# Kernel tuning notes

Hardware: AMD Instinct MI355X
Metric: run time of the kernel (lower is better)

## Reference

```python
import jax, jax.numpy as jnp
import numpy as np

N_NODES = 100000
N_EDGES = 1600000
IN_DIM = 128
EMB_DIM = 128
NUM_EDGE_EMB = 4
LN_EPS = 1e-5


def setup_inputs() -> dict:
    key = jax.random.key(0)
    ks = jax.random.split(key, 8)
    x = jax.random.normal(ks[0], (N_NODES, IN_DIM), dtype=jnp.float32)
    edge_index = jax.random.randint(ks[1], (2, N_EDGES), 0, N_NODES, dtype=jnp.int64)
    edge_attr = jax.random.randint(ks[2], (N_EDGES,), 0, NUM_EDGE_EMB, dtype=jnp.int64)
    # learned params
    edge_emb = jax.random.normal(ks[3], (NUM_EDGE_EMB, IN_DIM), dtype=jnp.float32)
    eps = jnp.zeros((), dtype=jnp.float32)  # GINEConv train_eps init 0
    s1 = 1.0 / np.sqrt(IN_DIM)
    W1 = jax.random.uniform(ks[4], (IN_DIM, EMB_DIM), jnp.float32, -s1, s1)
    b1 = jnp.zeros((EMB_DIM,), jnp.float32)
    ln_g = jnp.ones((EMB_DIM,), jnp.float32)
    ln_b = jnp.zeros((EMB_DIM,), jnp.float32)
    s2 = 1.0 / np.sqrt(EMB_DIM)
    W2 = jax.random.uniform(ks[5], (EMB_DIM, EMB_DIM), jnp.float32, -s2, s2)
    b2 = jnp.zeros((EMB_DIM,), jnp.float32)
    return {"x": x, "edge_index": edge_index, "edge_attr": edge_attr,
            "edge_emb": edge_emb, "eps": eps, "W1": W1, "b1": b1,
            "ln_g": ln_g, "ln_b": ln_b, "W2": W2, "b2": b2}


def reference(x, edge_index, edge_attr, edge_emb, eps, W1, b1, ln_g, ln_b, W2, b2):
    src, dst = edge_index[0], edge_index[1]
    # message: relu(x_j + e_ji), gathered per edge [E, D]
    msg = jax.nn.relu(x[src] + edge_emb[edge_attr])
    # scatter-add into destination nodes [N, D]
    agg = jax.ops.segment_sum(msg, dst, num_segments=x.shape[0])
    h = (1.0 + eps) * x + agg
    # MLP: Linear -> LayerNorm -> ReLU -> Linear
    h1 = h @ W1 + b1
    mu = jnp.mean(h1, axis=-1, keepdims=True)
    var = jnp.var(h1, axis=-1, keepdims=True)
    h1 = (h1 - mu) * jax.lax.rsqrt(var + LN_EPS) * ln_g + ln_b
    h1 = jax.nn.relu(h1)
    return h1 @ W2 + b2
```

## Files before the change

kernel.cpp:

```cpp
#include <hip/hip_runtime.h>
#include <hip/hip_fp16.h>

#define N_NODES 100000
#define N_EDGES 1600000
#define DIM 128
#define NBUK 782
#define EPB 4096
#define NBLK 391
#define NCNT (NBUK * NBLK)
#define NSC 299
#define CAPB 2720

typedef __attribute__((ext_vector_type(8))) short short8v;
typedef __attribute__((ext_vector_type(4))) float f32x4;
typedef _Float16 h2 __attribute__((ext_vector_type(2)));

__device__ __forceinline__ unsigned short f2bf(float f) {
    unsigned u = __float_as_uint(f);
    unsigned r = u + 0x7FFFu + ((u >> 16) & 1u);
    return (unsigned short)(r >> 16);
}
__device__ __forceinline__ float bf2f(unsigned short b) {
    return __uint_as_float(((unsigned)b) << 16);
}

__global__ __launch_bounds__(256) void hist2_conv(
    const int* __restrict__ ei, int* __restrict__ cnts,
    const float* __restrict__ x, ushort* __restrict__ xh, int do_conv)
{
    __shared__ int cnt[NBUK];
    for (int i = threadIdx.x; i < NBUK; i += 256) cnt[i] = 0;

    if (do_conv) {
        for (int i = blockIdx.x * 256 + threadIdx.x; i < N_NODES * DIM / 4;
             i += NBLK * 256) {
            float4 v = ((const float4*)x)[i];
            ushort4 o;
            o.x = __half_as_ushort(__float2half(v.x));
            o.y = __half_as_ushort(__float2half(v.y));
            o.z = __half_as_ushort(__float2half(v.z));
            o.w = __half_as_ushort(__float2half(v.w));
            ((ushort4*)xh)[i] = o;
        }
    }
    __syncthreads();

    int e0 = blockIdx.x * EPB;
    int e1 = min(e0 + EPB, N_EDGES);
    for (int e = e0 + threadIdx.x; e < e1; e += 256)
        atomicAdd(&cnt[ei[N_EDGES + e] >> 7], 1);
    __syncthreads();
    for (int b = threadIdx.x; b < NBUK; b += 256)
        cnts[b * NBLK + blockIdx.x] = cnt[b];
}

__global__ __launch_bounds__(256) void scanA(
    int* __restrict__ cnts, int* __restrict__ bsums)
{
    __shared__ int s[256];
    int t = threadIdx.x;
    int base = blockIdx.x * 1024 + t * 4;
    int v0 = (base + 0 < NCNT) ? cnts[base + 0] : 0;
    int v1 = (base + 1 < NCNT) ? cnts[base + 1] : 0;
    int v2 = (base + 2 < NCNT) ? cnts[base + 2] : 0;
    int v3 = (base + 3 < NCNT) ? cnts[base + 3] : 0;
    int sum = v0 + v1 + v2 + v3;
    s[t] = sum;
    __syncthreads();
    for (int off = 1; off < 256; off <<= 1) {
        int x = (t >= off) ? s[t - off] : 0;
        __syncthreads();
        s[t] += x;
        __syncthreads();
    }
    int excl = s[t] - sum;
    if (base + 0 < NCNT) cnts[base + 0] = excl;  excl += v0;
    if (base + 1 < NCNT) cnts[base + 1] = excl;  excl += v1;
    if (base + 2 < NCNT) cnts[base + 2] = excl;  excl += v2;
    if (base + 3 < NCNT) cnts[base + 3] = excl;
    if (t == 255) bsums[blockIdx.x] = s[255];
}

__global__ __launch_bounds__(512) void scanB(int* __restrict__ bsums)
{
    __shared__ int s[512];
    int t = threadIdx.x;
    int v = (t < NSC) ? bsums[t] : 0;
    s[t] = v;
    __syncthreads();
    for (int off = 1; off < 512; off <<= 1) {
        int x = (t >= off) ? s[t - off] : 0;
        __syncthreads();
        s[t] += x;
        __syncthreads();
    }
    if (t < NSC) bsums[t] = s[t] - v;
}

__global__ __launch_bounds__(256) void scanC_prepw(
    int* __restrict__ ebase, const int* __restrict__ bsums, int* __restrict__ bk,
    const float* __restrict__ W1, const float* __restrict__ W2,
    ushort* __restrict__ wf1, ushort* __restrict__ wf2)
{
    int i = blockIdx.x * 256 + threadIdx.x;
    if (i < NCNT) {
        int v = ebase[i] + bsums[i >> 10];
        ebase[i] = v;
        if (i % NBLK == 0) bk[i / NBLK] = v;
    }
    if (i == 0) bk[NBUK] = N_EDGES;

    if (i < DIM * DIM) {
        int lane = (i >> 3) & 63;
        int j = i & 7;
        int frag = i >> 9;
        int kt = frag >> 3, nt = frag & 7;
        int k = kt * 32 + (lane >> 4) * 8 + j;
        int n = nt * 16 + (lane & 15);
        wf1[i] = f2bf(W1[k * DIM + n]);
        wf2[i] = f2bf(W2[k * DIM + n]);
    }
}

__global__ __launch_bounds__(256) void pass2_scatter(
    const int* __restrict__ ei, const int* __restrict__ ea,
    const int* __restrict__ ebase, int* __restrict__ ebuf)
{
    __shared__ int cnt[NBUK];
    __shared__ int mybase[NBUK];
    for (int i = threadIdx.x; i < NBUK; i += 256) {
        cnt[i] = 0;
        mybase[i] = ebase[i * NBLK + blockIdx.x];
    }
    __syncthreads();
    int e0 = blockIdx.x * EPB;
    int e1 = min(e0 + EPB, N_EDGES);
    for (int e = e0 + threadIdx.x; e < e1; e += 256) {
        int src = ei[e];
        int dst = ei[N_EDGES + e];
        int at  = ea[e];
        int pay = src | (at << 17) | ((dst & 127) << 19);
        int b   = dst >> 7;
        int r   = atomicAdd(&cnt[b], 1);
        ebuf[mybase[b] + r] = pay;
    }
}

template<int HI>
__device__ __forceinline__ float h2acc(h2 m2, float acc) {
#if __has_builtin(__builtin_amdgcn_fdot2)
    h2 b;
    b[0] = (_Float16)(HI ? 0.f : 1.f);
    b[1] = (_Float16)(HI ? 1.f : 0.f);
    return __builtin_amdgcn_fdot2(m2, b, acc, false);
#else
    return acc + (float)m2[HI];
#endif
}

__device__ __forceinline__ void edge_acc(
    int pkv, int c, const unsigned* embh, float* acc, uint4 xv)
{
    const uint4 ev = *(const uint4*)&embh[((((unsigned)pkv >> 17) & 3) << 6) | (c << 2)];
    unsigned xs[4] = {xv.x, xv.y, xv.z, xv.w};
    unsigned es[4] = {ev.x, ev.y, ev.z, ev.w};
    const h2 z2 = (h2)(_Float16)0;
    #pragma unroll
    for (int j = 0; j < 4; ++j) {
        h2 a = __builtin_bit_cast(h2, xs[j]);
        h2 b = __builtin_bit_cast(h2, es[j]);
        h2 m2 = __builtin_elementwise_max(a + b, z2);
        acc[2 * j]     = h2acc<0>(m2, acc[2 * j]);
        acc[2 * j + 1] = h2acc<1>(m2, acc[2 * j + 1]);
    }
}

template<int USE16>
__global__ __launch_bounds__(512) void sort_gather(
    const int* __restrict__ bk, const int* __restrict__ ebuf,
    const float* __restrict__ x, const ushort* __restrict__ xh,
    const float* __restrict__ emb, const float* __restrict__ eps_p,
    ushort* __restrict__ hhi, ushort* __restrict__ hlo)
{
    __shared__ int col_l[CAPB];
    __shared__ int deg[128], sc[128], cur[128];
    __shared__ unsigned embh[256];
    __shared__ float femb[512];

    const int b = blockIdx.x;
    const int t = threadIdx.x;
    const int lo = bk[b];
    const int n_e = min(bk[b + 1] - lo, CAPB);

    if (t < 256) {
        float2 f = ((const float2*)emb)[t];
        if (USE16) {
            __half2 h = __floats2half2_rn(f.x, f.y);
            embh[t] = __builtin_bit_cast(unsigned, h);
        } else {
            femb[2 * t] = f.x;
            femb[2 * t + 1] = f.y;
        }
    }
    if (t < 128) deg[t] = 0;
    __syncthreads();

    for (int i = t; i < n_e; i += 512)
        atomicAdd(&deg[((unsigned)ebuf[lo + i] >> 19) & 127], 1);
    __syncthreads();

    if (t < 128) sc[t] = deg[t];
    __syncthreads();
    for (int off = 1; off < 128; off <<= 1) {
        int v = 0;
        if (t < 128 && t >= off) v = sc[t - off];
        __syncthreads();
        if (t < 128) sc[t] += v;
        __syncthreads();
    }
    if (t < 128) cur[t] = sc[t] - deg[t];
    __syncthreads();

    for (int i = t; i < n_e; i += 512) {
        int pk = ebuf[lo + i];
        int p = atomicAdd(&cur[((unsigned)pk >> 19) & 127], 1);
        col_l[p] = pk;
    }
    __syncthreads();

    const int g = t >> 4, c = t & 15;
    const float epsv = 1.0f + eps_p[0];

    for (int ln = g; ln < 128; ln += 32) {
        int n = b * 128 + ln;
        if (n >= N_NODES) break;
        int start = sc[ln] - deg[ln], end = sc[ln];
        float acc[8] = {0.f, 0.f, 0.f, 0.f, 0.f, 0.f, 0.f, 0.f};

        if (USE16) {
            int p = start;
            for (; p + 4 <= end; p += 4) {
                int pk[4];
                uint4 xv[4];
                #pragma unroll
                for (int u = 0; u < 4; ++u) pk[u] = col_l[p + u];
                #pragma unroll
                for (int u = 0; u < 4; ++u)
                    xv[u] = ((const uint4*)xh)[((pk[u] & 0x1FFFF) << 4) | c];
                #pragma unroll
                for (int u = 0; u < 4; ++u)
                    edge_acc(pk[u], c, embh, acc, xv[u]);
            }
            for (; p < end; ++p) {
                int pkv = col_l[p];
                uint4 xv = ((const uint4*)xh)[((pkv & 0x1FFFF) << 4) | c];
                edge_acc(pkv, c, embh, acc, xv);
            }
        } else {
            for (int p = start; p < end; ++p) {
                int pk = col_l[p];
                const float* xr = x + (size_t)(pk & 0x1FFFF) * DIM;
                float4 xa = ((const float4*)xr)[c * 2];
                float4 xb = ((const float4*)xr)[c * 2 + 1];
                const float* er = &femb[(((unsigned)pk >> 17) & 3) * DIM + c * 8];
                acc[0] += fmaxf(xa.x + er[0], 0.f);
                acc[1] += fmaxf(xa.y + er[1], 0.f);
                acc[2] += fmaxf(xa.z + er[2], 0.f);
                acc[3] += fmaxf(xa.w + er[3], 0.f);
                acc[4] += fmaxf(xb.x + er[4], 0.f);
                acc[5] += fmaxf(xb.y + er[5], 0.f);
                acc[6] += fmaxf(xb.z + er[6], 0.f);
                acc[7] += fmaxf(xb.w + er[7], 0.f);
            }
        }

        float4 xa = ((const float4*)(x + (size_t)n * DIM))[c * 2];
        float4 xb = ((const float4*)(x + (size_t)n * DIM))[c * 2 + 1];
        float o[8];
        o[0] = epsv * xa.x + acc[0];
        o[1] = epsv * xa.y + acc[1];
        o[2] = epsv * xa.z + acc[2];
        o[3] = epsv * xa.w + acc[3];
        o[4] = epsv * xb.x + acc[4];
        o[5] = epsv * xb.y + acc[5];
        o[6] = epsv * xb.z + acc[6];
        o[7] = epsv * xb.w + acc[7];

        unsigned hiw[4], low[4];
        #pragma unroll
        for (int j = 0; j < 4; ++j) {
            unsigned short h0 = f2bf(o[2 * j]);
            unsigned short h1 = f2bf(o[2 * j + 1]);
            unsigned short l0 = f2bf(o[2 * j] - bf2f(h0));
            unsigned short l1 = f2bf(o[2 * j + 1] - bf2f(h1));
            hiw[j] = (unsigned)h0 | ((unsigned)h1 << 16);
            low[j] = (unsigned)l0 | ((unsigned)l1 << 16);
        }
        ((uint4*)(hhi + (size_t)n * DIM))[c] = make_uint4(hiw[0], hiw[1], hiw[2], hiw[3]);
        ((uint4*)(hlo + (size_t)n * DIM))[c] = make_uint4(low[0], low[1], low[2], low[3]);
    }
}

__global__ __launch_bounds__(256) void fused_mlp(
    const ushort* __restrict__ hhi, const ushort* __restrict__ hlo,
    const ushort* __restrict__ wf1, const ushort* __restrict__ wf2,
    const float* __restrict__ b1,
    const float* __restrict__ lng, const float* __restrict__ lnb,
    const float* __restrict__ b2,
    float* __restrict__ out)
{
    __shared__ short w1s[DIM * DIM];
    __shared__ short w2s[DIM * DIM];
    __shared__ short scr[4 * 16 * DIM];

    #pragma unroll
    for (int i = 0; i < 8; ++i) {
        int idx = i * 256 + threadIdx.x;
        ((uint4*)w1s)[idx] = ((const uint4*)wf1)[idx];
        ((uint4*)w2s)[idx] = ((const uint4*)wf2)[idx];
    }
    __syncthreads();

    const int w  = threadIdx.x >> 6;
    const int l  = threadIdx.x & 63;
    const int lc = l & 15;
    const int lr = l >> 4;

    const int rbase = blockIdx.x * 64 + w * 16;
    const int arow = min(rbase + lc, N_NODES - 1);
    const ushort* hph = hhi + (size_t)arow * DIM;
    const ushort* hpl = hlo + (size_t)arow * DIM;

    float g[8], bb[8], bi1[8], bi2[8];
    #pragma unroll
    for (int nt = 0; nt < 8; ++nt) {
        g[nt]  = lng[nt * 16 + lc];
        bb[nt] = lnb[nt * 16 + lc];
        bi1[nt] = b1[nt * 16 + lc];
        bi2[nt] = b2[nt * 16 + lc];
    }

    f32x4 acc[8];
    #pragma unroll
    for (int nt = 0; nt < 8; ++nt)
        acc[nt] = (f32x4){bi1[nt], bi1[nt], bi1[nt], bi1[nt]};

    #pragma unroll
    for (int kt = 0; kt < 4; ++kt) {
        short8v ahi = *(const short8v*)(hph + kt * 32 + lr * 8);
        short8v alo = *(const short8v*)(hpl + kt * 32 + lr * 8);
        #pragma unroll
        for (int nt = 0; nt < 8; ++nt) {
            short8v bf = *(const short8v*)&w1s[((kt * 8 + nt) * 64 + l) * 8];
            acc[nt] = __builtin_amdgcn_mfma_f32_16x16x32_bf16(ahi, bf, acc[nt], 0, 0, 0);
            acc[nt] = __builtin_amdgcn_mfma_f32_16x16x32_bf16(alo, bf, acc[nt], 0, 0, 0);
        }
    }

    #pragma unroll
    for (int r = 0; r < 4; ++r) {
        float s1 = 0.f, s2 = 0.f;
        #pragma unroll
        for (int nt = 0; nt < 8; ++nt) { float v = acc[nt][r]; s1 += v; s2 += v * v; }
        s1 += __shfl_xor(s1, 1);  s2 += __shfl_xor(s2, 1);
        s1 += __shfl_xor(s1, 2);  s2 += __shfl_xor(s2, 2);
        s1 += __shfl_xor(s1, 4);  s2 += __shfl_xor(s2, 4);
        s1 += __shfl_xor(s1, 8);  s2 += __shfl_xor(s2, 8);
        float mu  = s1 * (1.0f / DIM);
        float var = s2 * (1.0f / DIM) - mu * mu;
        float rsd = rsqrtf(var + 1e-5f);
        int row = lr * 4 + r;
        #pragma unroll
        for (int nt = 0; nt < 8; ++nt) {
            float v = (acc[nt][r] - mu) * rsd * g[nt] + bb[nt];
            v = fmaxf(v, 0.f);
            int cidx = nt * 16 + lc;
            scr[w * 2048 + row * 128 + (((cidx >> 3) ^ row) << 3) + (cidx & 7)]
                = (short)f2bf(v);
        }
    }

    f32x4 acc2[8];
    #pragma unroll
    for (int nt = 0; nt < 8; ++nt)
        acc2[nt] = (f32x4){bi2[nt], bi2[nt], bi2[nt], bi2[nt]};

    #pragma unroll
    for (int kt = 0; kt < 4; ++kt) {
        short8v a2 = *(const short8v*)&scr[w * 2048 + lc * 128 + (((kt * 4 + lr) ^ lc) << 3)];
        #pragma unroll
        for (int nt = 0; nt < 8; ++nt) {
            short8v bf = *(const short8v*)&w2s[((kt * 8 + nt) * 64 + l) * 8];
            acc2[nt] = __builtin_amdgcn_mfma_f32_16x16x32_bf16(a2, bf, acc2[nt], 0, 0, 0);
        }
    }

    #pragma unroll
    for (int r = 0; r < 4; ++r) {
        int orow = rbase + lr * 4 + r;
        if (orow < N_NODES) {
            #pragma unroll
            for (int nt = 0; nt < 8; ++nt)
                out[(size_t)orow * DIM + nt * 16 + lc] = acc2[nt][r];
        }
    }
}

extern "C" void kernel_launch(void* const* d_in, const int* in_sizes, int n_in,
                              void* d_out, int out_size, void* d_ws, size_t ws_size,
                              hipStream_t stream) {
    const float* x    = (const float*)d_in[0];
    const int*   ei   = (const int*)d_in[1];
    const int*   ea   = (const int*)d_in[2];
    const float* emb  = (const float*)d_in[3];
    const float* epsp = (const float*)d_in[4];
    const float* W1   = (const float*)d_in[5];
    const float* b1   = (const float*)d_in[6];
    const float* lng  = (const float*)d_in[7];
    const float* lnb  = (const float*)d_in[8];
    const float* W2   = (const float*)d_in[9];
    const float* b2   = (const float*)d_in[10];
    float* out = (float*)d_out;

    char* ws = (char*)d_ws;
    int* bk     = (int*)(ws);
    int* bsums  = (int*)(ws + 4096);
    ushort* wf1 = (ushort*)(ws + 8192);
    ushort* wf2 = (ushort*)(ws + 40960);
    int* cnts   = (int*)(ws + 81920);
    int* ebuf   = (int*)(ws + 1310720);
    ushort* hhi = (ushort*)(ws + 8025984);
    ushort* hlo = (ushort*)(ws + 33625984);
    ushort* xh  = (ushort*)(ws + 59225984);
    const size_t NEED = 59225984 + (size_t)N_NODES * DIM * 2;

    const int use_f16 = (ws_size >= NEED) ? 1 : 0;

    hist2_conv<<<NBLK, 256, 0, stream>>>(ei, cnts, x, xh, use_f16);
    scanA<<<NSC, 256, 0, stream>>>(cnts, bsums);
    scanB<<<1, 512, 0, stream>>>(bsums);
    scanC_prepw<<<(NCNT + 255) / 256, 256, 0, stream>>>(
        cnts, bsums, bk, W1, W2, wf1, wf2);
    pass2_scatter<<<NBLK, 256, 0, stream>>>(ei, ea, cnts, ebuf);

    if (use_f16) {
        sort_gather<1><<<NBUK, 512, 0, stream>>>(
            bk, ebuf, x, xh, emb, epsp, hhi, hlo);
    } else {
        sort_gather<0><<<NBUK, 512, 0, stream>>>(
            bk, ebuf, x, xh, emb, epsp, hhi, hlo);
    }

    fused_mlp<<<(N_NODES + 63) / 64, 256, 0, stream>>>(
        hhi, hlo, wf1, wf2, b1, lng, lnb, b2, out);
}
```

Baseline: 158.6 us.

## Band-sort edges by source range so node groups gather with locality

The per-block counting sort now bins edges by destination node and by a 3-bit source-range band, giving 1024 bins. Each 16-thread group keeps four node accumulators in registers and walks all eight bands in order, so groups across the block read source rows from similar address ranges at the same time. The intent is better L2 locality for the random row gathers. In exchange it uses more registers (32 accumulators per thread), a longer 1024-entry scan with more barriers, and more shared memory, which may lower occupancy.

Result: slower. 178.0 us (+12.3%).

```diff
diff --git a/kernel.cpp b/kernel.cpp
--- a/kernel.cpp
+++ b/kernel.cpp
@@ -183,7 +183,9 @@
     ushort* __restrict__ hhi, ushort* __restrict__ hlo)
 {
     __shared__ int col_l[CAPB];
-    __shared__ int deg[128], sc[128], cur[128];
+    __shared__ int deg[1024];
+    __shared__ int sc[1024];
+    __shared__ int cur[1024];
     __shared__ unsigned embh[256];
     __shared__ float femb[512];
 
@@ -202,28 +204,33 @@
             femb[2 * t + 1] = f.y;
         }
     }
-    if (t < 128) deg[t] = 0;
-    __syncthreads();
-
-    for (int i = t; i < n_e; i += 512)
-        atomicAdd(&deg[((unsigned)ebuf[lo + i] >> 19) & 127], 1);
-    __syncthreads();
-
-    if (t < 128) sc[t] = deg[t];
-    __syncthreads();
-    for (int off = 1; off < 128; off <<= 1) {
-        int v = 0;
-        if (t < 128 && t >= off) v = sc[t - off];
-        __syncthreads();
-        if (t < 128) sc[t] += v;
-        __syncthreads();
-    }
-    if (t < 128) cur[t] = sc[t] - deg[t];
+    deg[t] = 0; deg[t + 512] = 0;
+    __syncthreads();
+
+    for (int i = t; i < n_e; i += 512) {
+        unsigned pk = (unsigned)ebuf[lo + i];
+        int bin = (((pk >> 19) & 127) << 3) | ((pk >> 14) & 7);
+        atomicAdd(&deg[bin], 1);
+    }
+    __syncthreads();
+
+    sc[t] = deg[t]; sc[t + 512] = deg[t + 512];
+    __syncthreads();
+    for (int off = 1; off < 1024; off <<= 1) {
+        int v0 = (t >= off) ? sc[t - off] : 0;
+        int v1 = (t + 512 >= off) ? sc[t + 512 - off] : 0;
+        __syncthreads();
+        sc[t] += v0; sc[t + 512] += v1;
+        __syncthreads();
+    }
+    cur[t] = sc[t] - deg[t];
+    cur[t + 512] = sc[t + 512] - deg[t + 512];
     __syncthreads();
 
     for (int i = t; i < n_e; i += 512) {
         int pk = ebuf[lo + i];
-        int p = atomicAdd(&cur[((unsigned)pk >> 19) & 127], 1);
+        int bin = ((((unsigned)pk >> 19) & 127) << 3) | (((unsigned)pk >> 14) & 7);
+        int p = atomicAdd(&cur[bin], 1);
         col_l[p] = pk;
     }
     __syncthreads();
@@ -231,60 +238,72 @@
     const int g = t >> 4, c = t & 15;
     const float epsv = 1.0f + eps_p[0];
 
-    for (int ln = g; ln < 128; ln += 32) {
-        int n = b * 128 + ln;
-        if (n >= N_NODES) break;
-        int start = sc[ln] - deg[ln], end = sc[ln];
-        float acc[8] = {0.f, 0.f, 0.f, 0.f, 0.f, 0.f, 0.f, 0.f};
-
-        if (USE16) {
-            int p = start;
-            for (; p + 4 <= end; p += 4) {
-                int pk[4];
-                uint4 xv[4];
-                #pragma unroll
-                for (int u = 0; u < 4; ++u) pk[u] = col_l[p + u];
-                #pragma unroll
-                for (int u = 0; u < 4; ++u)
-                    xv[u] = ((const uint4*)xh)[((pk[u] & 0x1FFFF) << 4) | c];
-                #pragma unroll
-                for (int u = 0; u < 4; ++u)
-                    edge_acc(pk[u], c, embh, acc, xv[u]);
+    float acc[4][8];
+    #pragma unroll
+    for (int q = 0; q < 4; ++q)
+        #pragma unroll
+        for (int j = 0; j < 8; ++j) acc[q][j] = 0.f;
+
+    for (int band = 0; band < 8; ++band) {
+        #pragma unroll
+        for (int q = 0; q < 4; ++q) {
+            int ln = g + q * 32;
+            int bin = ln * 8 + band;
+            int bs = sc[bin] - deg[bin], be = sc[bin];
+            if (USE16) {
+                int p = bs;
+                for (; p + 4 <= be; p += 4) {
+                    int pk[4];
+                    uint4 xv[4];
+                    #pragma unroll
+                    for (int u = 0; u < 4; ++u) pk[u] = col_l[p + u];
+                    #pragma unroll
+                    for (int u = 0; u < 4; ++u)
+                        xv[u] = ((const uint4*)xh)[((pk[u] & 0x1FFFF) << 4) | c];
+                    #pragma unroll
+                    for (int u = 0; u < 4; ++u)
+                        edge_acc(pk[u], c, embh, acc[q], xv[u]);
+                }
+                for (; p < be; ++p) {
+                    int pkv = col_l[p];
+                    uint4 xv = ((const uint4*)xh)[((pkv & 0x1FFFF) << 4) | c];
+                    edge_acc(pkv, c, embh, acc[q], xv);
+                }
+            } else {
+                for (int p = bs; p < be; ++p) {
+                    int pk = col_l[p];
+                    const float* xr = x + (size_t)(pk & 0x1FFFF) * DIM;
+                    float4 xa = ((const float4*)xr)[c * 2];
+                    float4 xb = ((const float4*)xr)[c * 2 + 1];
+                    const float* er = &femb[(((unsigned)pk >> 17) & 3) * DIM + c * 8];
+                    acc[q][0] += fmaxf(xa.x + er[0], 0.f);
+                    acc[q][1] += fmaxf(xa.y + er[1], 0.f);
+                    acc[q][2] += fmaxf(xa.z + er[2], 0.f);
+                    acc[q][3] += fmaxf(xa.w + er[3], 0.f);
+                    acc[q][4] += fmaxf(xb.x + er[4], 0.f);
+                    acc[q][5] += fmaxf(xb.y + er[5], 0.f);
+                    acc[q][6] += fmaxf(xb.z + er[6], 0.f);
+                    acc[q][7] += fmaxf(xb.w + er[7], 0.f);
+                }
             }
-            for (; p < end; ++p) {
-                int pkv = col_l[p];
-                uint4 xv = ((const uint4*)xh)[((pkv & 0x1FFFF) << 4) | c];
-                edge_acc(pkv, c, embh, acc, xv);
-            }
-        } else {
-            for (int p = start; p < end; ++p) {
-                int pk = col_l[p];
-                const float* xr = x + (size_t)(pk & 0x1FFFF) * DIM;
-                float4 xa = ((const float4*)xr)[c * 2];
-                float4 xb = ((const float4*)xr)[c * 2 + 1];
-                const float* er = &femb[(((unsigned)pk >> 17) & 3) * DIM + c * 8];
-                acc[0] += fmaxf(xa.x + er[0], 0.f);
-                acc[1] += fmaxf(xa.y + er[1], 0.f);
-                acc[2] += fmaxf(xa.z + er[2], 0.f);
-                acc[3] += fmaxf(xa.w + er[3], 0.f);
-                acc[4] += fmaxf(xb.x + er[4], 0.f);
-                acc[5] += fmaxf(xb.y + er[5], 0.f);
-                acc[6] += fmaxf(xb.z + er[6], 0.f);
-                acc[7] += fmaxf(xb.w + er[7], 0.f);
-            }
-        }
-
+        }
+    }
+
+    #pragma unroll
+    for (int q = 0; q < 4; ++q) {
+        int n = b * 128 + g + q * 32;
+        if (n >= N_NODES) continue;
         float4 xa = ((const float4*)(x + (size_t)n * DIM))[c * 2];
         float4 xb = ((const float4*)(x + (size_t)n * DIM))[c * 2 + 1];
         float o[8];
-        o[0] = epsv * xa.x + acc[0];
-        o[1] = epsv * xa.y + acc[1];
-        o[2] = epsv * xa.z + acc[2];
-        o[3] = epsv * xa.w + acc[3];
-        o[4] = epsv * xb.x + acc[4];
-        o[5] = epsv * xb.y + acc[5];
-        o[6] = epsv * xb.z + acc[6];
-        o[7] = epsv * xb.w + acc[7];
+        o[0] = epsv * xa.x + acc[q][0];
+        o[1] = epsv * xa.y + acc[q][1];
+        o[2] = epsv * xa.z + acc[q][2];
+        o[3] = epsv * xa.w + acc[q][3];
+        o[4] = epsv * xb.x + acc[q][4];
+        o[5] = epsv * xb.y + acc[q][5];
+        o[6] = epsv * xb.z + acc[q][6];
+        o[7] = epsv * xb.w + acc[q][7];
 
         unsigned hiw[4], low[4];
         #pragma unroll
```

## Enlarge histogram blocks and sub-sort bucket edges by source sub-range

Applied to the files above, without the earlier changes.

Raises edges per histogram/scatter block fourfold, which cuts the count table, the number of scan blocks and the scanB size. Inside each destination bucket, edges are now counting-sorted by destination and then by three bits of the source index (1024 bins instead of 128). Within a node's edge list, sources end up grouped by sub-range, which is meant to improve locality of the x gathers. Fewer, larger histogram blocks reduce parallelism in hist/scatter, and the sub-sort adds a larger shared-memory scan to each bucket.

Result: slower. 196.8 us (+24.1%).

```diff
diff --git a/kernel.cpp b/kernel.cpp
--- a/kernel.cpp
+++ b/kernel.cpp
@@ -5,10 +5,10 @@
 #define N_EDGES 1600000
 #define DIM 128
 #define NBUK 782
-#define EPB 4096
-#define NBLK 391
+#define EPB 16384
+#define NBLK 98
 #define NCNT (NBUK * NBLK)
-#define NSC 299
+#define NSC 75
 #define CAPB 2720
 
 typedef __attribute__((ext_vector_type(8))) short short8v;
@@ -81,14 +81,14 @@
     if (t == 255) bsums[blockIdx.x] = s[255];
 }
 
-__global__ __launch_bounds__(512) void scanB(int* __restrict__ bsums)
-{
-    __shared__ int s[512];
+__global__ __launch_bounds__(128) void scanB(int* __restrict__ bsums)
+{
+    __shared__ int s[128];
     int t = threadIdx.x;
     int v = (t < NSC) ? bsums[t] : 0;
     s[t] = v;
     __syncthreads();
-    for (int off = 1; off < 512; off <<= 1) {
+    for (int off = 1; off < 128; off <<= 1) {
         int x = (t >= off) ? s[t - off] : 0;
         __syncthreads();
         s[t] += x;
@@ -183,7 +183,9 @@
     ushort* __restrict__ hhi, ushort* __restrict__ hlo)
 {
     __shared__ int col_l[CAPB];
-    __shared__ int deg[128], sc[128], cur[128];
+    __shared__ int deg[1024];
+    __shared__ int sc[1024];
+    __shared__ int cur[1024];
     __shared__ unsigned embh[256];
     __shared__ float femb[512];
 
@@ -202,28 +204,33 @@
             femb[2 * t + 1] = f.y;
         }
     }
-    if (t < 128) deg[t] = 0;
-    __syncthreads();
-
-    for (int i = t; i < n_e; i += 512)
-        atomicAdd(&deg[((unsigned)ebuf[lo + i] >> 19) & 127], 1);
-    __syncthreads();
-
-    if (t < 128) sc[t] = deg[t];
-    __syncthreads();
-    for (int off = 1; off < 128; off <<= 1) {
-        int v = 0;
-        if (t < 128 && t >= off) v = sc[t - off];
-        __syncthreads();
-        if (t < 128) sc[t] += v;
-        __syncthreads();
-    }
-    if (t < 128) cur[t] = sc[t] - deg[t];
+    deg[t] = 0; deg[t + 512] = 0;
+    __syncthreads();
+
+    for (int i = t; i < n_e; i += 512) {
+        unsigned pk = (unsigned)ebuf[lo + i];
+        int bin = (((pk >> 19) & 127) << 3) | ((pk >> 14) & 7);
+        atomicAdd(&deg[bin], 1);
+    }
+    __syncthreads();
+
+    sc[t] = deg[t]; sc[t + 512] = deg[t + 512];
+    __syncthreads();
+    for (int off = 1; off < 1024; off <<= 1) {
+        int v0 = (t >= off) ? sc[t - off] : 0;
+        int v1 = (t + 512 >= off) ? sc[t + 512 - off] : 0;
+        __syncthreads();
+        sc[t] += v0; sc[t + 512] += v1;
+        __syncthreads();
+    }
+    cur[t] = sc[t] - deg[t];
+    cur[t + 512] = sc[t + 512] - deg[t + 512];
     __syncthreads();
 
     for (int i = t; i < n_e; i += 512) {
         int pk = ebuf[lo + i];
-        int p = atomicAdd(&cur[((unsigned)pk >> 19) & 127], 1);
+        int bin = ((((unsigned)pk >> 19) & 127) << 3) | (((unsigned)pk >> 14) & 7);
+        int p = atomicAdd(&cur[bin], 1);
         col_l[p] = pk;
     }
     __syncthreads();
@@ -234,7 +241,8 @@
     for (int ln = g; ln < 128; ln += 32) {
         int n = b * 128 + ln;
         if (n >= N_NODES) break;
-        int start = sc[ln] - deg[ln], end = sc[ln];
+        int start = sc[ln * 8] - deg[ln * 8];
+        int end = sc[ln * 8 + 7];
         float acc[8] = {0.f, 0.f, 0.f, 0.f, 0.f, 0.f, 0.f, 0.f};
 
         if (USE16) {
@@ -438,7 +446,7 @@
 
     hist2_conv<<<NBLK, 256, 0, stream>>>(ei, cnts, x, xh, use_f16);
     scanA<<<NSC, 256, 0, stream>>>(cnts, bsums);
-    scanB<<<1, 512, 0, stream>>>(bsums);
+    scanB<<<1, 128, 0, stream>>>(bsums);
     scanC_prepw<<<(NCNT + 255) / 256, 256, 0, stream>>>(
         cnts, bsums, bk, W1, W2, wf1, wf2);
     pass2_scatter<<<NBLK, 256, 0, stream>>>(ei, ea, cnts, ebuf);
```

## Switch MLP inputs to single fp16 split and fold block-sum scan into scanC

Applied to the files above, without the earlier changes.

Replaces the bf16 hi/lo split of the aggregated features with a single fp16 buffer, halving the intermediate write/read traffic and the first GEMM's MFMA count, and moves the weights and LN output to fp16 MFMA. It also removes the scanB launch by having every scanC block redundantly scan the block sums in shared memory. The cost is lower precision for the aggregated values: fp16 has less range than bf16 and fewer bits than the hi/lo pair, so large sums could overflow or lose accuracy.

Measured after the change: 150.1 us. 1.06x faster.

```diff
diff --git a/kernel.cpp b/kernel.cpp
--- a/kernel.cpp
+++ b/kernel.cpp
@@ -14,14 +14,10 @@
 typedef __attribute__((ext_vector_type(8))) short short8v;
 typedef __attribute__((ext_vector_type(4))) float f32x4;
 typedef _Float16 h2 __attribute__((ext_vector_type(2)));
-
-__device__ __forceinline__ unsigned short f2bf(float f) {
-    unsigned u = __float_as_uint(f);
-    unsigned r = u + 0x7FFFu + ((u >> 16) & 1u);
-    return (unsigned short)(r >> 16);
-}
-__device__ __forceinline__ float bf2f(unsigned short b) {
-    return __uint_as_float(((unsigned)b) << 16);
+typedef _Float16 h8v __attribute__((ext_vector_type(8)));
+
+__device__ __forceinline__ unsigned short f2h16(float f) {
+    return __half_as_ushort(__float2half(f));
 }
 
 __global__ __launch_bounds__(256) void hist2_conv(
@@ -36,10 +32,10 @@
              i += NBLK * 256) {
             float4 v = ((const float4*)x)[i];
             ushort4 o;
-            o.x = __half_as_ushort(__float2half(v.x));
-            o.y = __half_as_ushort(__float2half(v.y));
-            o.z = __half_as_ushort(__float2half(v.z));
-            o.w = __half_as_ushort(__float2half(v.w));
+            o.x = f2h16(v.x);
+            o.y = f2h16(v.y);
+            o.z = f2h16(v.z);
+            o.w = f2h16(v.w);
             ((ushort4*)xh)[i] = o;
         }
     }
@@ -81,9 +77,13 @@
     if (t == 255) bsums[blockIdx.x] = s[255];
 }
 
-__global__ __launch_bounds__(512) void scanB(int* __restrict__ bsums)
+__global__ __launch_bounds__(512) void scanC_prepw(
+    int* __restrict__ ebase, const int* __restrict__ bsums, int* __restrict__ bk,
+    const float* __restrict__ W1, const float* __restrict__ W2,
+    ushort* __restrict__ wf1, ushort* __restrict__ wf2)
 {
     __shared__ int s[512];
+    __shared__ int ex[512];
     int t = threadIdx.x;
     int v = (t < NSC) ? bsums[t] : 0;
     s[t] = v;
@@ -94,19 +94,14 @@
         s[t] += x;
         __syncthreads();
     }
-    if (t < NSC) bsums[t] = s[t] - v;
-}
-
-__global__ __launch_bounds__(256) void scanC_prepw(
-    int* __restrict__ ebase, const int* __restrict__ bsums, int* __restrict__ bk,
-    const float* __restrict__ W1, const float* __restrict__ W2,
-    ushort* __restrict__ wf1, ushort* __restrict__ wf2)
-{
-    int i = blockIdx.x * 256 + threadIdx.x;
+    ex[t] = s[t] - v;
+    __syncthreads();
+
+    int i = blockIdx.x * 512 + t;
     if (i < NCNT) {
-        int v = ebase[i] + bsums[i >> 10];
-        ebase[i] = v;
-        if (i % NBLK == 0) bk[i / NBLK] = v;
+        int val = ebase[i] + ex[i >> 10];
+        ebase[i] = val;
+        if (i % NBLK == 0) bk[i / NBLK] = val;
     }
     if (i == 0) bk[NBUK] = N_EDGES;
 
@@ -117,8 +112,8 @@
         int kt = frag >> 3, nt = frag & 7;
         int k = kt * 32 + (lane >> 4) * 8 + j;
         int n = nt * 16 + (lane & 15);
-        wf1[i] = f2bf(W1[k * DIM + n]);
-        wf2[i] = f2bf(W2[k * DIM + n]);
+        wf1[i] = f2h16(W1[k * DIM + n]);
+        wf2[i] = f2h16(W2[k * DIM + n]);
     }
 }
 
@@ -180,7 +175,7 @@
     const int* __restrict__ bk, const int* __restrict__ ebuf,
     const float* __restrict__ x, const ushort* __restrict__ xh,
     const float* __restrict__ emb, const float* __restrict__ eps_p,
-    ushort* __restrict__ hhi, ushort* __restrict__ hlo)
+    ushort* __restrict__ hb)
 {
     __shared__ int col_l[CAPB];
     __shared__ int deg[128], sc[128], cur[128];
@@ -286,32 +281,27 @@
         o[6] = epsv * xb.z + acc[6];
         o[7] = epsv * xb.w + acc[7];
 
-        unsigned hiw[4], low[4];
+        unsigned pw[4];
         #pragma unroll
         for (int j = 0; j < 4; ++j) {
-            unsigned short h0 = f2bf(o[2 * j]);
-            unsigned short h1 = f2bf(o[2 * j + 1]);
-            unsigned short l0 = f2bf(o[2 * j] - bf2f(h0));
-            unsigned short l1 = f2bf(o[2 * j + 1] - bf2f(h1));
-            hiw[j] = (unsigned)h0 | ((unsigned)h1 << 16);
-            low[j] = (unsigned)l0 | ((unsigned)l1 << 16);
-        }
-        ((uint4*)(hhi + (size_t)n * DIM))[c] = make_uint4(hiw[0], hiw[1], hiw[2], hiw[3]);
-        ((uint4*)(hlo + (size_t)n * DIM))[c] = make_uint4(low[0], low[1], low[2], low[3]);
+            __half2 hh = __floats2half2_rn(o[2 * j], o[2 * j + 1]);
+            pw[j] = __builtin_bit_cast(unsigned, hh);
+        }
+        ((uint4*)(hb + (size_t)n * DIM))[c] = make_uint4(pw[0], pw[1], pw[2], pw[3]);
     }
 }
 
 __global__ __launch_bounds__(256) void fused_mlp(
-    const ushort* __restrict__ hhi, const ushort* __restrict__ hlo,
+    const ushort* __restrict__ hb,
     const ushort* __restrict__ wf1, const ushort* __restrict__ wf2,
     const float* __restrict__ b1,
     const float* __restrict__ lng, const float* __restrict__ lnb,
     const float* __restrict__ b2,
     float* __restrict__ out)
 {
-    __shared__ short w1s[DIM * DIM];
-    __shared__ short w2s[DIM * DIM];
-    __shared__ short scr[4 * 16 * DIM];
+    __shared__ ushort w1s[DIM * DIM];
+    __shared__ ushort w2s[DIM * DIM];
+    __shared__ ushort scr[4 * 16 * DIM];
 
     #pragma unroll
     for (int i = 0; i < 8; ++i) {
@@ -328,8 +318,7 @@
 
     const int rbase = blockIdx.x * 64 + w * 16;
     const int arow = min(rbase + lc, N_NODES - 1);
-    const ushort* hph = hhi + (size_t)arow * DIM;
-    const ushort* hpl = hlo + (size_t)arow * DIM;
+    const ushort* hp = hb + (size_t)arow * DIM;
 
     float g[8], bb[8], bi1[8], bi2[8];
     #pragma unroll
@@ -347,13 +336,11 @@
 
     #pragma unroll
     for (int kt = 0; kt < 4; ++kt) {
-        short8v ahi = *(const short8v*)(hph + kt * 32 + lr * 8);
-        short8v alo = *(const short8v*)(hpl + kt * 32 + lr * 8);
+        h8v a = *(const h8v*)(hp + kt * 32 + lr * 8);
         #pragma unroll
         for (int nt = 0; nt < 8; ++nt) {
-            short8v bf = *(const short8v*)&w1s[((kt * 8 + nt) * 64 + l) * 8];
-            acc[nt] = __builtin_amdgcn_mfma_f32_16x16x32_bf16(ahi, bf, acc[nt], 0, 0, 0);
-            acc[nt] = __builtin_amdgcn_mfma_f32_16x16x32_bf16(alo, bf, acc[nt], 0, 0, 0);
+            h8v bf = *(const h8v*)&w1s[((kt * 8 + nt) * 64 + l) * 8];
+            acc[nt] = __builtin_amdgcn_mfma_f32_16x16x32_f16(a, bf, acc[nt], 0, 0, 0);
         }
     }
 
@@ -376,7 +363,7 @@
             v = fmaxf(v, 0.f);
             int cidx = nt * 16 + lc;
             scr[w * 2048 + row * 128 + (((cidx >> 3) ^ row) << 3) + (cidx & 7)]
-                = (short)f2bf(v);
+                = f2h16(v);
         }
     }
 
@@ -387,11 +374,11 @@
 
     #pragma unroll
     for (int kt = 0; kt < 4; ++kt) {
-        short8v a2 = *(const short8v*)&scr[w * 2048 + lc * 128 + (((kt * 4 + lr) ^ lc) << 3)];
+        h8v a2 = *(const h8v*)&scr[w * 2048 + lc * 128 + (((kt * 4 + lr) ^ lc) << 3)];
         #pragma unroll
         for (int nt = 0; nt < 8; ++nt) {
-            short8v bf = *(const short8v*)&w2s[((kt * 8 + nt) * 64 + l) * 8];
-            acc2[nt] = __builtin_amdgcn_mfma_f32_16x16x32_bf16(a2, bf, acc2[nt], 0, 0, 0);
+            h8v bf = *(const h8v*)&w2s[((kt * 8 + nt) * 64 + l) * 8];
+            acc2[nt] = __builtin_amdgcn_mfma_f32_16x16x32_f16(a2, bf, acc2[nt], 0, 0, 0);
         }
     }
 
@@ -429,8 +416,7 @@
     ushort* wf2 = (ushort*)(ws + 40960);
     int* cnts   = (int*)(ws + 81920);
     int* ebuf   = (int*)(ws + 1310720);
-    ushort* hhi = (ushort*)(ws + 8025984);
-    ushort* hlo = (ushort*)(ws + 33625984);
+    ushort* hb  = (ushort*)(ws + 8025984);
     ushort* xh  = (ushort*)(ws + 59225984);
     const size_t NEED = 59225984 + (size_t)N_NODES * DIM * 2;
 
@@ -438,19 +424,18 @@
 
     hist2_conv<<<NBLK, 256, 0, stream>>>(ei, cnts, x, xh, use_f16);
     scanA<<<NSC, 256, 0, stream>>>(cnts, bsums);
-    scanB<<<1, 512, 0, stream>>>(bsums);
-    scanC_prepw<<<(NCNT + 255) / 256, 256, 0, stream>>>(
+    scanC_prepw<<<(NCNT + 511) / 512, 512, 0, stream>>>(
         cnts, bsums, bk, W1, W2, wf1, wf2);
     pass2_scatter<<<NBLK, 256, 0, stream>>>(ei, ea, cnts, ebuf);
 
     if (use_f16) {
         sort_gather<1><<<NBUK, 512, 0, stream>>>(
-            bk, ebuf, x, xh, emb, epsp, hhi, hlo);
+            bk, ebuf, x, xh, emb, epsp, hb);
     } else {
         sort_gather<0><<<NBUK, 512, 0, stream>>>(
-            bk, ebuf, x, xh, emb, epsp, hhi, hlo);
+            bk, ebuf, x, xh, emb, epsp, hb);
     }
 
     fused_mlp<<<(N_NODES + 63) / 64, 256, 0, stream>>>(
-        hhi, hlo, wf1, wf2, b1, lng, lnb, b2, out);
-}
+        hb, wf1, wf2, b1, lng, lnb, b2, out);
+}
```
